# Kernel optimization log

Measured on AMD Instinct MI355X. Metric: run time of the kernel, lower is better.

The kernel has to match this reference:

```python
import math
import jax
import jax.numpy as jnp
import numpy as np

H = 16
D_MODEL = 1024
D_K = D_MODEL // H            # 64
POS_DK = D_MODEL // 4 // H    # 16
EMB_DIM = D_MODEL // 4        # 256
MAX_DIST = 1000
RES = 20                      # RealEmbedding discretization resolution (3rd ctor arg)
N_EMB = 2 * MAX_DIST * RES + 1
B, NQ, NK = 2, 512, 512


def setup_inputs() -> dict:
    key0 = jax.random.key(0)
    ks = jax.random.split(key0, 16)
    s = 0.02

    def lin(k, din, dout):
        return (jax.random.normal(k, (din, dout), jnp.float32) * s,
                jnp.zeros((dout,), jnp.float32))

    Wq, bq = lin(ks[7], D_MODEL, D_MODEL)
    Wk, bk = lin(ks[8], D_MODEL, D_MODEL)
    Wv, bv = lin(ks[9], D_MODEL, D_MODEL)
    Wo, bo = lin(ks[10], D_MODEL, D_MODEL)
    Wb, bb = lin(ks[11], POS_DK, 1)
    return {
        "query": jax.random.normal(ks[0], (B, NQ, D_MODEL), jnp.float32),
        "key": jax.random.normal(ks[1], (B, NK, D_MODEL), jnp.float32),
        "value": jax.random.normal(ks[2], (B, NK, D_MODEL), jnp.float32),
        "query_x": jax.random.uniform(ks[3], (B, NQ), jnp.float32, 0.0, float(MAX_DIST)),
        "query_y": jax.random.uniform(ks[4], (B, NQ), jnp.float32, 0.0, float(MAX_DIST)),
        "key_x": jax.random.uniform(ks[5], (B, NK), jnp.float32, 0.0, float(MAX_DIST)),
        "key_y": jax.random.uniform(ks[6], (B, NK), jnp.float32, 0.0, float(MAX_DIST)),
        "Wq": Wq, "bq": bq, "Wk": Wk, "bk": bk, "Wv": Wv, "bv": bv,
        "Wo": Wo, "bo": bo,
        "x_table": jax.random.normal(ks[12], (N_EMB, EMB_DIM), jnp.float32) * s,
        "y_table": jax.random.normal(ks[13], (N_EMB, EMB_DIM), jnp.float32) * s,
        "Wb": Wb, "bb": bb,
    }


def _real_emb(table, d):
    # RealEmbedding: clamp real-valued distance to [-MAX_DIST, MAX_DIST],
    # discretize at resolution RES, nearest-neighbor table lookup.
    idx = jnp.round((jnp.clip(d, -MAX_DIST, MAX_DIST) + MAX_DIST) * RES).astype(jnp.int32)
    return table[idx]


def _forward(query, key, value, query_x, query_y, key_x, key_y,
             Wq, bq, Wk, bk, Wv, bv, Wo, bo, x_table, y_table, Wb, bb):
    b, nq, _ = query.shape
    nk = key.shape[1]
    # relative-position differences, layout (b, nk, nq) exactly as the torch expand
    x_diff = query_x[:, None, :] - key_x[:, :, None]
    y_diff = query_y[:, None, :] - key_y[:, :, None]
    pos_emb = _real_emb(x_table, x_diff) + _real_emb(y_table, y_diff)  # (b, nk, nq, EMB_DIM)
    pos_emb = pos_emb.reshape(b, nk, nq, H, POS_DK)
    att_bias = jax.nn.sigmoid((pos_emb @ Wb + bb)[..., 0])  # (b, nk, nq, H)
    # permute(0,3,1,2): (b, H, nk, nq); added to (b, H, nq, nk) scores (self-attn, nq==nk)
    att_bias = att_bias.transpose(0, 3, 1, 2)
    q = (query @ Wq + bq).reshape(b, nq, H, D_K).transpose(0, 2, 1, 3)
    k = (key @ Wk + bk).reshape(b, nk, H, D_K).transpose(0, 2, 1, 3)
    v = (value @ Wv + bv).reshape(b, nk, H, D_K).transpose(0, 2, 1, 3)
    scores = jnp.einsum('bhqd,bhkd->bhqk', q, k) / math.sqrt(D_K) + att_bias
    p_attn = jax.nn.softmax(scores, axis=-1)  # dropout p=0 / eval mode
    out = jnp.einsum('bhqk,bhkd->bhqd', p_attn, v)
    out = out.transpose(0, 2, 1, 3).reshape(b, nq, D_MODEL)
    return out @ Wo + bo


def reference(query, key, value, query_x, query_y, key_x, key_y,
              Wq, bq, Wk, bk, Wv, bv, Wo, bo, x_table, y_table, Wb, bb):
    return _forward(query, key, value, query_x, query_y, key_x, key_y,
                    Wq, bq, Wk, bk, Wv, bv, Wo, bo, x_table, y_table, Wb, bb)
```

## Files before the change

kernel.cpp:

```cpp
#include <hip/hip_runtime.h>
#include <math.h>

#define HH 16
#define DM 1024
#define DK 64
#define NE 40001
#define NB 2
#define NQS 512
#define NKS 512

typedef unsigned short ushort_t;
typedef __attribute__((ext_vector_type(8))) short short8v;
typedef __attribute__((ext_vector_type(4))) float f32x4;

__device__ __forceinline__ ushort_t f2bf(float f) {
    union { float f; unsigned u; } v; v.f = f;
    unsigned r = v.u + 0x7FFFu + ((v.u >> 16) & 1u);
    return (ushort_t)(r >> 16);
}
__device__ __forceinline__ unsigned pack2(float a, float b) {
    return (unsigned)f2bf(a) | ((unsigned)f2bf(b) << 16);
}
__device__ __forceinline__ float asf(unsigned u) {
    union { unsigned u; float f; } v; v.u = u; return v.f;
}

__global__ __launch_bounds__(256) void cvt_k(
    const float* __restrict__ xq, const float* __restrict__ xk, const float* __restrict__ xv,
    const float* __restrict__ wq, const float* __restrict__ wk,
    const float* __restrict__ wv, const float* __restrict__ wo,
    ushort_t* __restrict__ qc, ushort_t* __restrict__ kc, ushort_t* __restrict__ vc,
    ushort_t* __restrict__ wqt, ushort_t* __restrict__ wkt,
    ushort_t* __restrict__ wvt, ushort_t* __restrict__ wot)
{
    const int z = blockIdx.z;
    const int t = blockIdx.x * 256 + threadIdx.x;
    if (z < 3) {
        const float* src = (z == 0) ? xq : ((z == 1) ? xk : xv);
        ushort_t* dst = (z == 0) ? qc : ((z == 1) ? kc : vc);
        float4 a = ((const float4*)src)[t * 2];
        float4 b = ((const float4*)src)[t * 2 + 1];
        uint4 o;
        o.x = pack2(a.x, a.y); o.y = pack2(a.z, a.w);
        o.z = pack2(b.x, b.y); o.w = pack2(b.z, b.w);
        *reinterpret_cast<uint4*>(dst + t * 8) = o;
    } else {
        const float* w = (z == 3) ? wq : ((z == 4) ? wk : ((z == 5) ? wv : wo));
        ushort_t* wt = (z == 3) ? wqt : ((z == 4) ? wkt : ((z == 5) ? wvt : wot));
        const int n = t & 1023;
        const int k0 = (t >> 10) << 3;
        float e[8];
#pragma unroll
        for (int j = 0; j < 8; ++j) e[j] = w[(k0 + j) * 1024 + n];
        uint4 o;
        o.x = pack2(e[0], e[1]); o.y = pack2(e[2], e[3]);
        o.z = pack2(e[4], e[5]); o.w = pack2(e[6], e[7]);
        *reinterpret_cast<uint4*>(wt + n * 1024 + k0) = o;
    }
}

__global__ __launch_bounds__(256) void proj_tables_k(
    const float* __restrict__ xt, const float* __restrict__ yt,
    const float* __restrict__ Wb,
    float* __restrict__ xproj, float* __restrict__ yproj)
{
    int gid = blockIdx.x * 256 + threadIdx.x;
    const int tot = NE * HH;
    if (gid >= 2 * tot) return;
    const float* tab = xt;
    float* dst = xproj;
    int r = gid;
    if (r >= tot) { r -= tot; tab = yt; dst = yproj; }
    int i = r >> 4, h = r & 15;
    const float* p = tab + i * 256 + h * 16;
    float s = 0.f;
#pragma unroll
    for (int d = 0; d < 16; ++d) s += p[d] * Wb[d];
    dst[r] = s;
}

__global__ __launch_bounds__(256) void bias_k(
    const float* __restrict__ xproj, const float* __restrict__ yproj,
    const float* __restrict__ qx, const float* __restrict__ qy,
    const float* __restrict__ kx, const float* __restrict__ ky,
    const float* __restrict__ bbp,
    ushort_t* __restrict__ biasf)
{
    const int t = threadIdx.x;
    const int qt = blockIdx.x, kt = blockIdx.y, b = blockIdx.z;
    const int ql = t & 15, kl = t >> 4;
    const int qg = qt * 16 + ql, kg = kt * 16 + kl;

    float dx = qx[b * NKS + kg] - kx[b * NQS + qg];
    float dy = qy[b * NKS + kg] - ky[b * NQS + qg];
    int ix = (int)rintf((fminf(fmaxf(dx, -1000.f), 1000.f) + 1000.f) * 20.f);
    int iy = (int)rintf((fminf(fmaxf(dy, -1000.f), 1000.f) + 1000.f) * 20.f);
    const float bb = bbp[0];

    const float4* xr = (const float4*)(xproj + ix * 16);
    const float4* yr = (const float4*)(yproj + iy * 16);
    float xa[16], ya[16];
#pragma unroll
    for (int c = 0; c < 4; ++c) {
        float4 xv = xr[c], yv = yr[c];
        xa[c * 4 + 0] = xv.x; xa[c * 4 + 1] = xv.y; xa[c * 4 + 2] = xv.z; xa[c * 4 + 3] = xv.w;
        ya[c * 4 + 0] = yv.x; ya[c * 4 + 1] = yv.y; ya[c * 4 + 2] = yv.z; ya[c * 4 + 3] = yv.w;
    }
    const int lane_j = ((kl >> 2) * 16 + ql) * 4 + (kl & 3);
    const int tile_stride = 32 * 32 * 256;
#pragma unroll
    for (int h = 0; h < HH; ++h) {
        float t2 = xa[h] + ya[h] + bb;
        float sig = 1.f / (1.f + __expf(-t2));
        biasf[((b * HH + h) * 32 + kt) * (32 * 256) + qt * 256 + lane_j] = f2bf(sig);
    }
    (void)tile_stride;
}

template<int EPI>
__global__ __launch_bounds__(256) void gemm_bf16_k(
    const ushort_t* __restrict__ A0, const ushort_t* __restrict__ A1, const ushort_t* __restrict__ A2,
    const ushort_t* __restrict__ B0, const ushort_t* __restrict__ B1, const ushort_t* __restrict__ B2,
    const float* __restrict__ bi0, const float* __restrict__ bi1, const float* __restrict__ bi2,
    ushort_t* __restrict__ Yh0, ushort_t* __restrict__ Yh1, ushort_t* __restrict__ Yh2,
    float* __restrict__ Yf)
{
    __shared__ ushort_t As[64][40];
    __shared__ ushort_t Bs[64][40];
    const int z = blockIdx.z;
    const ushort_t* A = (z == 0) ? A0 : ((z == 1) ? A1 : A2);
    const ushort_t* B = (z == 0) ? B0 : ((z == 1) ? B1 : B2);
    const float* bi = (z == 0) ? bi0 : ((z == 1) ? bi1 : bi2);
    ushort_t* Yh = (z == 0) ? Yh0 : ((z == 1) ? Yh1 : Yh2);
    const int m0 = blockIdx.y * 64, n0 = blockIdx.x * 64;
    const int tid = threadIdx.x;
    const int lane = tid & 63, w = tid >> 6;
    const int wm = w >> 1, wn = w & 1;
    const int sr = tid >> 2, sc = (tid & 3) * 8;

    f32x4 acc[2][2] = {};
    short8v ar = *(const short8v*)(A + (m0 + sr) * 1024 + sc);
    short8v br = *(const short8v*)(B + (n0 + sr) * 1024 + sc);

    const int fr = lane & 15;
    const int ko = (lane >> 4) * 8;

    for (int k0 = 0; k0 < 1024; k0 += 32) {
        __syncthreads();
        *reinterpret_cast<short8v*>(&As[sr][sc]) = ar;
        *reinterpret_cast<short8v*>(&Bs[sr][sc]) = br;
        __syncthreads();
        if (k0 + 32 < 1024) {
            ar = *(const short8v*)(A + (m0 + sr) * 1024 + k0 + 32 + sc);
            br = *(const short8v*)(B + (n0 + sr) * 1024 + k0 + 32 + sc);
        }
        short8v af0 = *(const short8v*)&As[wm * 32 + fr][ko];
        short8v af1 = *(const short8v*)&As[wm * 32 + 16 + fr][ko];
        short8v bf0 = *(const short8v*)&Bs[wn * 32 + fr][ko];
        short8v bf1 = *(const short8v*)&Bs[wn * 32 + 16 + fr][ko];
        acc[0][0] = __builtin_amdgcn_mfma_f32_16x16x32_bf16(af0, bf0, acc[0][0], 0, 0, 0);
        acc[0][1] = __builtin_amdgcn_mfma_f32_16x16x32_bf16(af0, bf1, acc[0][1], 0, 0, 0);
        acc[1][0] = __builtin_amdgcn_mfma_f32_16x16x32_bf16(af1, bf0, acc[1][0], 0, 0, 0);
        acc[1][1] = __builtin_amdgcn_mfma_f32_16x16x32_bf16(af1, bf1, acc[1][1], 0, 0, 0);
    }

    const int cr = (lane >> 4) * 4;
    const int cc = lane & 15;
#pragma unroll
    for (int m = 0; m < 2; ++m) {
#pragma unroll
        for (int n = 0; n < 2; ++n) {
            int grow = m0 + wm * 32 + m * 16 + cr;
            int gcol = n0 + wn * 32 + n * 16 + cc;
            float bv = bi[gcol];
            if (EPI == 0) {
#pragma unroll
                for (int j = 0; j < 4; ++j)
                    Yf[(grow + j) * 1024 + gcol] = acc[m][n][j] + bv;
            } else {
                int hh = gcol >> 6, dd = gcol & 63;
                if (z != 2) {
#pragma unroll
                    for (int j = 0; j < 4; ++j) {
                        int r = grow + j, bb_ = r >> 9, nn = r & 511;
                        Yh[((bb_ * HH + hh) * NQS + nn) * DK + dd] = f2bf(acc[m][n][j] + bv);
                    }
                } else {
#pragma unroll
                    for (int j = 0; j < 4; ++j) {
                        int r = grow + j, bb_ = r >> 9, nn = r & 511;
                        Yh[((bb_ * HH + hh) * DK + dd) * NKS + nn] = f2bf(acc[m][n][j] + bv);
                    }
                }
            }
        }
    }
}

__global__ __launch_bounds__(256, 4) void attn_k(
    const ushort_t* __restrict__ qbh, const ushort_t* __restrict__ kbh,
    const ushort_t* __restrict__ vtb, const ushort_t* __restrict__ biasf,
    ushort_t* __restrict__ attb)
{
    __shared__ ushort_t pst[4][16][40];
    __shared__ float obuf[4][16][76];
    __shared__ float mt[4][16], lt[4][16];

    const int tid = threadIdx.x;
    const int wid = tid >> 6, lane = tid & 63;
    const int q = lane & 15, g = lane >> 4;
    const int qt = blockIdx.x;
    const int h = blockIdx.y, b = blockIdx.z;
    const int bh = b * HH + h;

    const ushort_t* Qp = qbh + (bh * NQS + qt * 16 + q) * DK + g * 8;
    short8v qf0 = *(const short8v*)Qp;
    short8v qf1 = *(const short8v*)(Qp + 32);

    f32x4 oacc[4] = {};
    float m = -1e30f, l = 0.f;

#pragma unroll 2
    for (int c = 0; c < 4; ++c) {
        const int kc = wid * 128 + c * 32;
        const ushort_t* Kp = kbh + (bh * NKS + kc + q) * DK + g * 8;
        short8v kf00 = *(const short8v*)(Kp);
        short8v kf01 = *(const short8v*)(Kp + 32);
        short8v kf10 = *(const short8v*)(Kp + 16 * DK);
        short8v kf11 = *(const short8v*)(Kp + 16 * DK + 32);

        f32x4 s0 = {0.f, 0.f, 0.f, 0.f};
        f32x4 s1 = {0.f, 0.f, 0.f, 0.f};
        s0 = __builtin_amdgcn_mfma_f32_16x16x32_bf16(kf00, qf0, s0, 0, 0, 0);
        s0 = __builtin_amdgcn_mfma_f32_16x16x32_bf16(kf01, qf1, s0, 0, 0, 0);
        s1 = __builtin_amdgcn_mfma_f32_16x16x32_bf16(kf10, qf0, s1, 0, 0, 0);
        s1 = __builtin_amdgcn_mfma_f32_16x16x32_bf16(kf11, qf1, s1, 0, 0, 0);

        const int kt = kc >> 4;
        uint2 b0 = *((const uint2*)(biasf + ((bh * 32 + kt) * 32 + qt) * 256) + lane);
        uint2 b1 = *((const uint2*)(biasf + ((bh * 32 + kt + 1) * 32 + qt) * 256) + lane);

        float sv[8];
        sv[0] = s0[0] * 0.125f + asf(b0.x << 16);
        sv[1] = s0[1] * 0.125f + asf(b0.x & 0xFFFF0000u);
        sv[2] = s0[2] * 0.125f + asf(b0.y << 16);
        sv[3] = s0[3] * 0.125f + asf(b0.y & 0xFFFF0000u);
        sv[4] = s1[0] * 0.125f + asf(b1.x << 16);
        sv[5] = s1[1] * 0.125f + asf(b1.x & 0xFFFF0000u);
        sv[6] = s1[2] * 0.125f + asf(b1.y << 16);
        sv[7] = s1[3] * 0.125f + asf(b1.y & 0xFFFF0000u);

        float mc = fmaxf(fmaxf(fmaxf(sv[0], sv[1]), fmaxf(sv[2], sv[3])),
                         fmaxf(fmaxf(sv[4], sv[5]), fmaxf(sv[6], sv[7])));
        mc = fmaxf(mc, __shfl_xor(mc, 16));
        mc = fmaxf(mc, __shfl_xor(mc, 32));
        float mn = fmaxf(m, mc);

        float p[8], ps = 0.f;
#pragma unroll
        for (int j = 0; j < 8; ++j) { p[j] = __expf(sv[j] - mn); ps += p[j]; }
        float sc = __expf(m - mn);
        l = l * sc + ps;
        m = mn;
#pragma unroll
        for (int dt = 0; dt < 4; ++dt)
#pragma unroll
            for (int j = 0; j < 4; ++j) oacc[dt][j] *= sc;

        ushort_t* prow = &pst[wid][q][0];
        *(unsigned*)(prow + 4 * g)      = pack2(p[0], p[1]);
        *(unsigned*)(prow + 4 * g + 2)  = pack2(p[2], p[3]);
        *(unsigned*)(prow + 16 + 4 * g)     = pack2(p[4], p[5]);
        *(unsigned*)(prow + 16 + 4 * g + 2) = pack2(p[6], p[7]);
        short8v pf = *(const short8v*)&pst[wid][q][8 * g];

        const ushort_t* Vp = vtb + (bh * DK + q) * NKS + kc + g * 8;
#pragma unroll
        for (int dt = 0; dt < 4; ++dt) {
            short8v vf = *(const short8v*)(Vp + dt * 16 * NKS);
            oacc[dt] = __builtin_amdgcn_mfma_f32_16x16x32_bf16(vf, pf, oacc[dt], 0, 0, 0);
        }
    }

    float lr = l + __shfl_xor(l, 16);
    lr = lr + __shfl_xor(lr, 32);
    if (lane < 16) { mt[wid][lane] = m; lt[wid][lane] = lr; }
#pragma unroll
    for (int dt = 0; dt < 4; ++dt)
#pragma unroll
        for (int j = 0; j < 4; ++j)
            obuf[wid][q][dt * 16 + 4 * g + j] = oacc[dt][j];
    __syncthreads();

    const int mq = tid >> 4, d4 = (tid & 15) * 4;
    float m0 = mt[0][mq], m1 = mt[1][mq], m2 = mt[2][mq], m3 = mt[3][mq];
    float ms = fmaxf(fmaxf(m0, m1), fmaxf(m2, m3));
    float e0 = __expf(m0 - ms), e1 = __expf(m1 - ms);
    float e2 = __expf(m2 - ms), e3 = __expf(m3 - ms);
    float denom = lt[0][mq] * e0 + lt[1][mq] * e1 + lt[2][mq] * e2 + lt[3][mq] * e3;
    float inv = 1.f / denom;
    float4 o0 = *(float4*)&obuf[0][mq][d4];
    float4 o1 = *(float4*)&obuf[1][mq][d4];
    float4 o2 = *(float4*)&obuf[2][mq][d4];
    float4 o3 = *(float4*)&obuf[3][mq][d4];
    float r0 = (o0.x * e0 + o1.x * e1 + o2.x * e2 + o3.x * e3) * inv;
    float r1 = (o0.y * e0 + o1.y * e1 + o2.y * e2 + o3.y * e3) * inv;
    float r2 = (o0.z * e0 + o1.z * e1 + o2.z * e2 + o3.z * e3) * inv;
    float r3 = (o0.w * e0 + o1.w * e1 + o2.w * e2 + o3.w * e3) * inv;
    uint2 ow;
    ow.x = pack2(r0, r1); ow.y = pack2(r2, r3);
    *reinterpret_cast<uint2*>(attb + (b * NQS + qt * 16 + mq) * DM + h * DK + d4) = ow;
}

extern "C" void kernel_launch(void* const* d_in, const int* in_sizes, int n_in,
                              void* d_out, int out_size, void* d_ws, size_t ws_size,
                              hipStream_t stream)
{
    const float* query = (const float*)d_in[0];
    const float* key   = (const float*)d_in[1];
    const float* value = (const float*)d_in[2];
    const float* qx    = (const float*)d_in[3];
    const float* qy    = (const float*)d_in[4];
    const float* kx    = (const float*)d_in[5];
    const float* ky    = (const float*)d_in[6];
    const float* Wq    = (const float*)d_in[7];
    const float* bq    = (const float*)d_in[8];
    const float* Wk    = (const float*)d_in[9];
    const float* bk    = (const float*)d_in[10];
    const float* Wv    = (const float*)d_in[11];
    const float* bv    = (const float*)d_in[12];
    const float* Wo    = (const float*)d_in[13];
    const float* bo    = (const float*)d_in[14];
    const float* xt    = (const float*)d_in[15];
    const float* yt    = (const float*)d_in[16];
    const float* Wb    = (const float*)d_in[17];
    const float* bbp   = (const float*)d_in[18];
    float* out = (float*)d_out;

    float* ws = (float*)d_ws;
    float* xproj = ws;
    float* yproj = xproj + 640064;
    ushort_t* biasf = (ushort_t*)(yproj + 640064);
    float* p = yproj + 640064 + 4194304;
    ushort_t* qbh  = (ushort_t*)p;
    ushort_t* kbh  = (ushort_t*)(p + 524288);
    ushort_t* vtb  = (ushort_t*)(p + 2 * 524288);
    ushort_t* attb = (ushort_t*)(p + 3 * 524288);
    ushort_t* qc   = (ushort_t*)(p + 4 * 524288);
    ushort_t* kcb  = (ushort_t*)(p + 5 * 524288);
    ushort_t* vcb  = (ushort_t*)(p + 6 * 524288);
    ushort_t* wqt  = (ushort_t*)(p + 7 * 524288);
    ushort_t* wkt  = (ushort_t*)(p + 8 * 524288);
    ushort_t* wvt  = (ushort_t*)(p + 9 * 524288);
    ushort_t* wot  = (ushort_t*)(p + 10 * 524288);

    cvt_k<<<dim3(512, 1, 7), dim3(256), 0, stream>>>(
        query, key, value, Wq, Wk, Wv, Wo, qc, kcb, vcb, wqt, wkt, wvt, wot);
    proj_tables_k<<<dim3((2 * NE * HH + 255) / 256), dim3(256), 0, stream>>>(
        xt, yt, Wb, xproj, yproj);
    bias_k<<<dim3(32, 32, 2), dim3(256), 0, stream>>>(
        xproj, yproj, qx, qy, kx, ky, bbp, biasf);
    gemm_bf16_k<1><<<dim3(16, 16, 3), dim3(256), 0, stream>>>(
        qc, kcb, vcb, wqt, wkt, wvt, bq, bk, bv, qbh, kbh, vtb, nullptr);
    attn_k<<<dim3(32, 16, 2), dim3(256), 0, stream>>>(
        qbh, kbh, vtb, biasf, attb);
    gemm_bf16_k<0><<<dim3(16, 16, 1), dim3(256), 0, stream>>>(
        attb, attb, attb, wot, wot, wot, bo, bo, bo, nullptr, nullptr, nullptr, out);
}
```

Before: 96.21 us.

## Fuse activation bf16 conversion into QKV GEMM, widen K tile, shrink bias tables

The QKV projection GEMM now loads fp32 activations directly and packs them to bf16 while staging into shared memory, so the separate activation conversion pass and its workspace round trip are gone. The GEMM K-step is doubled to 64 with wider shared tiles, which halves the number of barrier pairs. The projected position tables are stored as bf16 instead of fp32, halving gather traffic in the bias kernel, and the 1/sqrt(dk) scale is folded into the K projection epilogue. Storing the tables in bf16 and pre-scaling K add extra rounding error.

```diff
diff --git a/kernel.cpp b/kernel.cpp
--- a/kernel.cpp
+++ b/kernel.cpp
@@ -26,61 +26,54 @@
 }
 
 __global__ __launch_bounds__(256) void cvt_k(
-    const float* __restrict__ xq, const float* __restrict__ xk, const float* __restrict__ xv,
     const float* __restrict__ wq, const float* __restrict__ wk,
     const float* __restrict__ wv, const float* __restrict__ wo,
-    ushort_t* __restrict__ qc, ushort_t* __restrict__ kc, ushort_t* __restrict__ vc,
     ushort_t* __restrict__ wqt, ushort_t* __restrict__ wkt,
     ushort_t* __restrict__ wvt, ushort_t* __restrict__ wot)
 {
     const int z = blockIdx.z;
     const int t = blockIdx.x * 256 + threadIdx.x;
-    if (z < 3) {
-        const float* src = (z == 0) ? xq : ((z == 1) ? xk : xv);
-        ushort_t* dst = (z == 0) ? qc : ((z == 1) ? kc : vc);
-        float4 a = ((const float4*)src)[t * 2];
-        float4 b = ((const float4*)src)[t * 2 + 1];
-        uint4 o;
-        o.x = pack2(a.x, a.y); o.y = pack2(a.z, a.w);
-        o.z = pack2(b.x, b.y); o.w = pack2(b.z, b.w);
-        *reinterpret_cast<uint4*>(dst + t * 8) = o;
-    } else {
-        const float* w = (z == 3) ? wq : ((z == 4) ? wk : ((z == 5) ? wv : wo));
-        ushort_t* wt = (z == 3) ? wqt : ((z == 4) ? wkt : ((z == 5) ? wvt : wot));
-        const int n = t & 1023;
-        const int k0 = (t >> 10) << 3;
-        float e[8];
-#pragma unroll
-        for (int j = 0; j < 8; ++j) e[j] = w[(k0 + j) * 1024 + n];
-        uint4 o;
-        o.x = pack2(e[0], e[1]); o.y = pack2(e[2], e[3]);
-        o.z = pack2(e[4], e[5]); o.w = pack2(e[6], e[7]);
-        *reinterpret_cast<uint4*>(wt + n * 1024 + k0) = o;
-    }
+    const float* w = (z == 0) ? wq : ((z == 1) ? wk : ((z == 2) ? wv : wo));
+    ushort_t* wt = (z == 0) ? wqt : ((z == 1) ? wkt : ((z == 2) ? wvt : wot));
+    const int n = t & 1023;
+    const int k0 = (t >> 10) << 3;
+    float e[8];
+#pragma unroll
+    for (int j = 0; j < 8; ++j) e[j] = w[(k0 + j) * 1024 + n];
+    uint4 o;
+    o.x = pack2(e[0], e[1]); o.y = pack2(e[2], e[3]);
+    o.z = pack2(e[4], e[5]); o.w = pack2(e[6], e[7]);
+    *reinterpret_cast<uint4*>(wt + n * 1024 + k0) = o;
 }
 
 __global__ __launch_bounds__(256) void proj_tables_k(
     const float* __restrict__ xt, const float* __restrict__ yt,
     const float* __restrict__ Wb,
-    float* __restrict__ xproj, float* __restrict__ yproj)
+    ushort_t* __restrict__ xproj, ushort_t* __restrict__ yproj)
 {
     int gid = blockIdx.x * 256 + threadIdx.x;
     const int tot = NE * HH;
     if (gid >= 2 * tot) return;
     const float* tab = xt;
-    float* dst = xproj;
+    ushort_t* dst = xproj;
     int r = gid;
     if (r >= tot) { r -= tot; tab = yt; dst = yproj; }
     int i = r >> 4, h = r & 15;
-    const float* p = tab + i * 256 + h * 16;
-    float s = 0.f;
-#pragma unroll
-    for (int d = 0; d < 16; ++d) s += p[d] * Wb[d];
-    dst[r] = s;
+    const float4* p = (const float4*)(tab + i * 256 + h * 16);
+    float4 w0 = *(const float4*)(Wb);
+    float4 w1 = *(const float4*)(Wb + 4);
+    float4 w2 = *(const float4*)(Wb + 8);
+    float4 w3 = *(const float4*)(Wb + 12);
+    float4 p0 = p[0], p1 = p[1], p2 = p[2], p3 = p[3];
+    float s = p0.x * w0.x + p0.y * w0.y + p0.z * w0.z + p0.w * w0.w
+            + p1.x * w1.x + p1.y * w1.y + p1.z * w1.z + p1.w * w1.w
+            + p2.x * w2.x + p2.y * w2.y + p2.z * w2.z + p2.w * w2.w
+            + p3.x * w3.x + p3.y * w3.y + p3.z * w3.z + p3.w * w3.w;
+    dst[r] = f2bf(s);
 }
 
 __global__ __launch_bounds__(256) void bias_k(
-    const float* __restrict__ xproj, const float* __restrict__ yproj,
+    const ushort_t* __restrict__ xproj, const ushort_t* __restrict__ yproj,
     const float* __restrict__ qx, const float* __restrict__ qy,
     const float* __restrict__ kx, const float* __restrict__ ky,
     const float* __restrict__ bbp,
@@ -97,71 +90,111 @@
     int iy = (int)rintf((fminf(fmaxf(dy, -1000.f), 1000.f) + 1000.f) * 20.f);
     const float bb = bbp[0];
 
-    const float4* xr = (const float4*)(xproj + ix * 16);
-    const float4* yr = (const float4*)(yproj + iy * 16);
+    uint4 xw0 = *(const uint4*)(xproj + ix * 16);
+    uint4 xw1 = *(const uint4*)(xproj + ix * 16 + 8);
+    uint4 yw0 = *(const uint4*)(yproj + iy * 16);
+    uint4 yw1 = *(const uint4*)(yproj + iy * 16 + 8);
+
     float xa[16], ya[16];
-#pragma unroll
-    for (int c = 0; c < 4; ++c) {
-        float4 xv = xr[c], yv = yr[c];
-        xa[c * 4 + 0] = xv.x; xa[c * 4 + 1] = xv.y; xa[c * 4 + 2] = xv.z; xa[c * 4 + 3] = xv.w;
-        ya[c * 4 + 0] = yv.x; ya[c * 4 + 1] = yv.y; ya[c * 4 + 2] = yv.z; ya[c * 4 + 3] = yv.w;
+    {
+        unsigned u[8] = {xw0.x, xw0.y, xw0.z, xw0.w, xw1.x, xw1.y, xw1.z, xw1.w};
+        unsigned v[8] = {yw0.x, yw0.y, yw0.z, yw0.w, yw1.x, yw1.y, yw1.z, yw1.w};
+#pragma unroll
+        for (int wv = 0; wv < 8; ++wv) {
+            xa[2 * wv]     = asf(u[wv] << 16);
+            xa[2 * wv + 1] = asf(u[wv] & 0xFFFF0000u);
+            ya[2 * wv]     = asf(v[wv] << 16);
+            ya[2 * wv + 1] = asf(v[wv] & 0xFFFF0000u);
+        }
     }
     const int lane_j = ((kl >> 2) * 16 + ql) * 4 + (kl & 3);
-    const int tile_stride = 32 * 32 * 256;
 #pragma unroll
     for (int h = 0; h < HH; ++h) {
         float t2 = xa[h] + ya[h] + bb;
         float sig = 1.f / (1.f + __expf(-t2));
         biasf[((b * HH + h) * 32 + kt) * (32 * 256) + qt * 256 + lane_j] = f2bf(sig);
     }
-    (void)tile_stride;
 }
 
 template<int EPI>
 __global__ __launch_bounds__(256) void gemm_bf16_k(
-    const ushort_t* __restrict__ A0, const ushort_t* __restrict__ A1, const ushort_t* __restrict__ A2,
+    const void* __restrict__ A0v, const void* __restrict__ A1v, const void* __restrict__ A2v,
     const ushort_t* __restrict__ B0, const ushort_t* __restrict__ B1, const ushort_t* __restrict__ B2,
     const float* __restrict__ bi0, const float* __restrict__ bi1, const float* __restrict__ bi2,
     ushort_t* __restrict__ Yh0, ushort_t* __restrict__ Yh1, ushort_t* __restrict__ Yh2,
     float* __restrict__ Yf)
 {
-    __shared__ ushort_t As[64][40];
-    __shared__ ushort_t Bs[64][40];
+    __shared__ ushort_t As[64][72];
+    __shared__ ushort_t Bs[64][72];
     const int z = blockIdx.z;
-    const ushort_t* A = (z == 0) ? A0 : ((z == 1) ? A1 : A2);
-    const ushort_t* B = (z == 0) ? B0 : ((z == 1) ? B1 : B2);
+    const void* Av = (z == 0) ? A0v : ((z == 1) ? A1v : A2v);
+    const float* Af = (const float*)Av;
+    const ushort_t* Ah = (const ushort_t*)Av;
+    const ushort_t* Bp = (z == 0) ? B0 : ((z == 1) ? B1 : B2);
     const float* bi = (z == 0) ? bi0 : ((z == 1) ? bi1 : bi2);
     ushort_t* Yh = (z == 0) ? Yh0 : ((z == 1) ? Yh1 : Yh2);
     const int m0 = blockIdx.y * 64, n0 = blockIdx.x * 64;
     const int tid = threadIdx.x;
     const int lane = tid & 63, w = tid >> 6;
     const int wm = w >> 1, wn = w & 1;
-    const int sr = tid >> 2, sc = (tid & 3) * 8;
+    const int srow = tid >> 2, scg = (tid & 3) * 16;
 
     f32x4 acc[2][2] = {};
-    short8v ar = *(const short8v*)(A + (m0 + sr) * 1024 + sc);
-    short8v br = *(const short8v*)(B + (n0 + sr) * 1024 + sc);
+    float4 arf0, arf1, arf2, arf3;
+    uint4 arh0, arh1, brh0, brh1;
+
+    auto loadA = [&](int kk) {
+        if (EPI) {
+            const float* ap = Af + (m0 + srow) * 1024 + kk + scg;
+            arf0 = *(const float4*)(ap);
+            arf1 = *(const float4*)(ap + 4);
+            arf2 = *(const float4*)(ap + 8);
+            arf3 = *(const float4*)(ap + 12);
+        } else {
+            const ushort_t* ap = Ah + (m0 + srow) * 1024 + kk + scg;
+            arh0 = *(const uint4*)(ap);
+            arh1 = *(const uint4*)(ap + 8);
+        }
+    };
+    auto loadB = [&](int kk) {
+        const ushort_t* bp = Bp + (n0 + srow) * 1024 + kk + scg;
+        brh0 = *(const uint4*)(bp);
+        brh1 = *(const uint4*)(bp + 8);
+    };
+    loadA(0); loadB(0);
 
     const int fr = lane & 15;
     const int ko = (lane >> 4) * 8;
 
-    for (int k0 = 0; k0 < 1024; k0 += 32) {
+    for (int k0 = 0; k0 < 1024; k0 += 64) {
         __syncthreads();
-        *reinterpret_cast<short8v*>(&As[sr][sc]) = ar;
-        *reinterpret_cast<short8v*>(&Bs[sr][sc]) = br;
+        if (EPI) {
+            uint4 w0, w1;
+            w0.x = pack2(arf0.x, arf0.y); w0.y = pack2(arf0.z, arf0.w);
+            w0.z = pack2(arf1.x, arf1.y); w0.w = pack2(arf1.z, arf1.w);
+            w1.x = pack2(arf2.x, arf2.y); w1.y = pack2(arf2.z, arf2.w);
+            w1.z = pack2(arf3.x, arf3.y); w1.w = pack2(arf3.z, arf3.w);
+            *(uint4*)&As[srow][scg]     = w0;
+            *(uint4*)&As[srow][scg + 8] = w1;
+        } else {
+            *(uint4*)&As[srow][scg]     = arh0;
+            *(uint4*)&As[srow][scg + 8] = arh1;
+        }
+        *(uint4*)&Bs[srow][scg]     = brh0;
+        *(uint4*)&Bs[srow][scg + 8] = brh1;
         __syncthreads();
-        if (k0 + 32 < 1024) {
-            ar = *(const short8v*)(A + (m0 + sr) * 1024 + k0 + 32 + sc);
-            br = *(const short8v*)(B + (n0 + sr) * 1024 + k0 + 32 + sc);
-        }
-        short8v af0 = *(const short8v*)&As[wm * 32 + fr][ko];
-        short8v af1 = *(const short8v*)&As[wm * 32 + 16 + fr][ko];
-        short8v bf0 = *(const short8v*)&Bs[wn * 32 + fr][ko];
-        short8v bf1 = *(const short8v*)&Bs[wn * 32 + 16 + fr][ko];
-        acc[0][0] = __builtin_amdgcn_mfma_f32_16x16x32_bf16(af0, bf0, acc[0][0], 0, 0, 0);
-        acc[0][1] = __builtin_amdgcn_mfma_f32_16x16x32_bf16(af0, bf1, acc[0][1], 0, 0, 0);
-        acc[1][0] = __builtin_amdgcn_mfma_f32_16x16x32_bf16(af1, bf0, acc[1][0], 0, 0, 0);
-        acc[1][1] = __builtin_amdgcn_mfma_f32_16x16x32_bf16(af1, bf1, acc[1][1], 0, 0, 0);
+        if (k0 + 64 < 1024) { loadA(k0 + 64); loadB(k0 + 64); }
+#pragma unroll
+        for (int ks = 0; ks < 64; ks += 32) {
+            short8v af0 = *(const short8v*)&As[wm * 32 + fr][ks + ko];
+            short8v af1 = *(const short8v*)&As[wm * 32 + 16 + fr][ks + ko];
+            short8v bf0 = *(const short8v*)&Bs[wn * 32 + fr][ks + ko];
+            short8v bf1 = *(const short8v*)&Bs[wn * 32 + 16 + fr][ks + ko];
+            acc[0][0] = __builtin_amdgcn_mfma_f32_16x16x32_bf16(af0, bf0, acc[0][0], 0, 0, 0);
+            acc[0][1] = __builtin_amdgcn_mfma_f32_16x16x32_bf16(af0, bf1, acc[0][1], 0, 0, 0);
+            acc[1][0] = __builtin_amdgcn_mfma_f32_16x16x32_bf16(af1, bf0, acc[1][0], 0, 0, 0);
+            acc[1][1] = __builtin_amdgcn_mfma_f32_16x16x32_bf16(af1, bf1, acc[1][1], 0, 0, 0);
+        }
     }
 
     const int cr = (lane >> 4) * 4;
@@ -179,11 +212,17 @@
                     Yf[(grow + j) * 1024 + gcol] = acc[m][n][j] + bv;
             } else {
                 int hh = gcol >> 6, dd = gcol & 63;
-                if (z != 2) {
+                if (z == 0) {
 #pragma unroll
                     for (int j = 0; j < 4; ++j) {
                         int r = grow + j, bb_ = r >> 9, nn = r & 511;
                         Yh[((bb_ * HH + hh) * NQS + nn) * DK + dd] = f2bf(acc[m][n][j] + bv);
+                    }
+                } else if (z == 1) {
+#pragma unroll
+                    for (int j = 0; j < 4; ++j) {
+                        int r = grow + j, bb_ = r >> 9, nn = r & 511;
+                        Yh[((bb_ * HH + hh) * NQS + nn) * DK + dd] = f2bf((acc[m][n][j] + bv) * 0.125f);
                     }
                 } else {
 #pragma unroll
@@ -241,14 +280,14 @@
         uint2 b1 = *((const uint2*)(biasf + ((bh * 32 + kt + 1) * 32 + qt) * 256) + lane);
 
         float sv[8];
-        sv[0] = s0[0] * 0.125f + asf(b0.x << 16);
-        sv[1] = s0[1] * 0.125f + asf(b0.x & 0xFFFF0000u);
-        sv[2] = s0[2] * 0.125f + asf(b0.y << 16);
-        sv[3] = s0[3] * 0.125f + asf(b0.y & 0xFFFF0000u);
-        sv[4] = s1[0] * 0.125f + asf(b1.x << 16);
-        sv[5] = s1[1] * 0.125f + asf(b1.x & 0xFFFF0000u);
-        sv[6] = s1[2] * 0.125f + asf(b1.y << 16);
-        sv[7] = s1[3] * 0.125f + asf(b1.y & 0xFFFF0000u);
+        sv[0] = s0[0] + asf(b0.x << 16);
+        sv[1] = s0[1] + asf(b0.x & 0xFFFF0000u);
+        sv[2] = s0[2] + asf(b0.y << 16);
+        sv[3] = s0[3] + asf(b0.y & 0xFFFF0000u);
+        sv[4] = s1[0] + asf(b1.x << 16);
+        sv[5] = s1[1] + asf(b1.x & 0xFFFF0000u);
+        sv[6] = s1[2] + asf(b1.y << 16);
+        sv[7] = s1[3] + asf(b1.y & 0xFFFF0000u);
 
         float mc = fmaxf(fmaxf(fmaxf(sv[0], sv[1]), fmaxf(sv[2], sv[3])),
                          fmaxf(fmaxf(sv[4], sv[5]), fmaxf(sv[6], sv[7])));
@@ -268,8 +307,8 @@
             for (int j = 0; j < 4; ++j) oacc[dt][j] *= sc;
 
         ushort_t* prow = &pst[wid][q][0];
-        *(unsigned*)(prow + 4 * g)      = pack2(p[0], p[1]);
-        *(unsigned*)(prow + 4 * g + 2)  = pack2(p[2], p[3]);
+        *(unsigned*)(prow + 4 * g)          = pack2(p[0], p[1]);
+        *(unsigned*)(prow + 4 * g + 2)      = pack2(p[2], p[3]);
         *(unsigned*)(prow + 16 + 4 * g)     = pack2(p[4], p[5]);
         *(unsigned*)(prow + 16 + 4 * g + 2) = pack2(p[6], p[7]);
         short8v pf = *(const short8v*)&pst[wid][q][8 * g];
@@ -337,31 +376,26 @@
     const float* bbp   = (const float*)d_in[18];
     float* out = (float*)d_out;
 
-    float* ws = (float*)d_ws;
-    float* xproj = ws;
-    float* yproj = xproj + 640064;
-    ushort_t* biasf = (ushort_t*)(yproj + 640064);
-    float* p = yproj + 640064 + 4194304;
-    ushort_t* qbh  = (ushort_t*)p;
-    ushort_t* kbh  = (ushort_t*)(p + 524288);
-    ushort_t* vtb  = (ushort_t*)(p + 2 * 524288);
-    ushort_t* attb = (ushort_t*)(p + 3 * 524288);
-    ushort_t* qc   = (ushort_t*)(p + 4 * 524288);
-    ushort_t* kcb  = (ushort_t*)(p + 5 * 524288);
-    ushort_t* vcb  = (ushort_t*)(p + 6 * 524288);
-    ushort_t* wqt  = (ushort_t*)(p + 7 * 524288);
-    ushort_t* wkt  = (ushort_t*)(p + 8 * 524288);
-    ushort_t* wvt  = (ushort_t*)(p + 9 * 524288);
-    ushort_t* wot  = (ushort_t*)(p + 10 * 524288);
-
-    cvt_k<<<dim3(512, 1, 7), dim3(256), 0, stream>>>(
-        query, key, value, Wq, Wk, Wv, Wo, qc, kcb, vcb, wqt, wkt, wvt, wot);
+    ushort_t* xprojh = (ushort_t*)d_ws;
+    ushort_t* yprojh = xprojh + 640064;
+    ushort_t* biasf  = yprojh + 640064;
+    ushort_t* qbh    = biasf + 8388608;
+    ushort_t* kbh    = qbh + 1048576;
+    ushort_t* vtb    = kbh + 1048576;
+    ushort_t* attb   = vtb + 1048576;
+    ushort_t* wqt    = attb + 1048576;
+    ushort_t* wkt    = wqt + 1048576;
+    ushort_t* wvt    = wkt + 1048576;
+    ushort_t* wot    = wvt + 1048576;
+
+    cvt_k<<<dim3(512, 1, 4), dim3(256), 0, stream>>>(
+        Wq, Wk, Wv, Wo, wqt, wkt, wvt, wot);
     proj_tables_k<<<dim3((2 * NE * HH + 255) / 256), dim3(256), 0, stream>>>(
-        xt, yt, Wb, xproj, yproj);
+        xt, yt, Wb, xprojh, yprojh);
     bias_k<<<dim3(32, 32, 2), dim3(256), 0, stream>>>(
-        xproj, yproj, qx, qy, kx, ky, bbp, biasf);
+        xprojh, yprojh, qx, qy, kx, ky, bbp, biasf);
     gemm_bf16_k<1><<<dim3(16, 16, 3), dim3(256), 0, stream>>>(
-        qc, kcb, vcb, wqt, wkt, wvt, bq, bk, bv, qbh, kbh, vtb, nullptr);
+        query, key, value, wqt, wkt, wvt, bq, bk, bv, qbh, kbh, vtb, nullptr);
     attn_k<<<dim3(32, 16, 2), dim3(256), 0, stream>>>(
         qbh, kbh, vtb, biasf, attb);
     gemm_bf16_k<0><<<dim3(16, 16, 1), dim3(256), 0, stream>>>(
```

Result: faster. 92.58 us (-3.8%).
